# Optimization experiments

Measured on AMD Instinct MI355X. Metric: run time of the kernel, lower is better.

## Reference

```python
import jax, jax.numpy as jnp
import numpy as np

EMBED_DIM = 768
NUM_HEADS = 8
HEAD_DIM = EMBED_DIM // NUM_HEADS
SCALE = HEAD_DIM ** -0.5
B = 256
N_TOTAL = 16384


def setup_inputs() -> dict:
    key = jax.random.key(0)
    ks = jax.random.split(key, 10)
    s = 1.0 / np.sqrt(EMBED_DIM)
    inp = {
        "query": jax.random.normal(ks[0], (B, EMBED_DIM), jnp.float32),
        "search": jax.random.normal(ks[1], (N_TOTAL, EMBED_DIM), jnp.float32),
        # q_proj / k_proj: Linear(embed_dim, embed_dim)
        "Wq": jax.random.uniform(ks[2], (EMBED_DIM, EMBED_DIM), jnp.float32, -s, s),
        "bq": jax.random.uniform(ks[3], (EMBED_DIM,), jnp.float32, -s, s),
        "Wk": jax.random.uniform(ks[4], (EMBED_DIM, EMBED_DIM), jnp.float32, -s, s),
        "bk": jax.random.uniform(ks[5], (EMBED_DIM,), jnp.float32, -s, s),
        # score_fusion: Linear(H, H//2) -> GELU -> Linear(H//2, 1)
        "W1": jax.random.uniform(ks[6], (NUM_HEADS // 2, NUM_HEADS), jnp.float32, -1.0 / np.sqrt(NUM_HEADS), 1.0 / np.sqrt(NUM_HEADS)),
        "b1": jax.random.uniform(ks[7], (NUM_HEADS // 2,), jnp.float32, -1.0 / np.sqrt(NUM_HEADS), 1.0 / np.sqrt(NUM_HEADS)),
        "W2": jax.random.uniform(ks[8], (1, NUM_HEADS // 2), jnp.float32, -1.0 / np.sqrt(NUM_HEADS // 2), 1.0 / np.sqrt(NUM_HEADS // 2)),
        "b2": jax.random.uniform(ks[9], (1,), jnp.float32, -1.0 / np.sqrt(NUM_HEADS // 2), 1.0 / np.sqrt(NUM_HEADS // 2)),
    }
    return inp


def reference(query, search, Wq, bq, Wk, bk, W1, b1, W2, b2):
    Bq = query.shape[0]
    Nt = search.shape[0]
    # projections -> (B, H, hd) and (N, H, hd)
    q = (query @ Wq.T + bq).reshape(Bq, NUM_HEADS, HEAD_DIM)
    k = (search @ Wk.T + bk).reshape(Nt, NUM_HEADS, HEAD_DIM)
    # per-head dot products: (B, N, H)
    attn_logits = jnp.einsum('bhd,nhd->bnh', q, k) * SCALE
    # tiny MLP over head axis: H -> H//2 -> 1, exact (erf) GELU as in torch default
    h = jax.nn.gelu(attn_logits @ W1.T + b1, approximate=False)
    scores = h @ W2.T + b2  # (B, N, 1)
    return scores.squeeze(-1)
```

## Files before the change

kernel.cpp:

```cpp
#include <hip/hip_runtime.h>
#include <math.h>

#define SCALE 0.1020620726159658f

typedef __attribute__((ext_vector_type(8))) short shortx8;
typedef __attribute__((ext_vector_type(4))) float floatx4;

__device__ __forceinline__ float bf2f(unsigned short u) {
  union { unsigned int i; float f; } c; c.i = ((unsigned int)u) << 16; return c.f;
}
__device__ __forceinline__ unsigned short f2bf(float f) {
  union { float f; unsigned int i; } c; c.f = f;
  unsigned int x = c.i;
  x += 0x7fffu + ((x >> 16) & 1u);
  return (unsigned short)(x >> 16);
}
__device__ __forceinline__ float geluf(float x) {
  return 0.5f * x * (1.0f + erff(x * 0.70710678118654752f));
}
__device__ __forceinline__ float lde(const void* p, long i, int fp32) {
  return fp32 ? ((const float*)p)[i] : bf2f(((const unsigned short*)p)[i]);
}

__global__ void detect_dtype(const unsigned short* __restrict__ s, int* __restrict__ flag) {
  int t = threadIdx.x;
  int big = 0;
  for (int i = t; i < 256; i += 64) {
    int e = (s[i] >> 7) & 0xFF;
    if (e >= 160) big = 1;
  }
  unsigned long long m = __ballot(big);
  if (t == 0) *flag = (m != 0ULL) ? 1 : 0;
}

__global__ void convert_in(const void* __restrict__ q, const void* __restrict__ wq,
                           unsigned short* __restrict__ qb, unsigned short* __restrict__ wqb,
                           const int* __restrict__ flagp) {
  int fl = *flagp;
  int idx = blockIdx.x * 256 + threadIdx.x;
  const int n1 = 196608;
  if (idx < n1) {
    qb[idx] = fl ? f2bf(((const float*)q)[idx]) : ((const unsigned short*)q)[idx];
  } else {
    int j = idx - n1;
    wqb[j] = fl ? f2bf(((const float*)wq)[j]) : ((const unsigned short*)wq)[j];
  }
}

__global__ void transpose_bf(const void* __restrict__ in, unsigned short* __restrict__ out,
                             const int* __restrict__ flagp) {
  int fl = *flagp;
  __shared__ unsigned short tile[32][33];
  int tx = threadIdx.x, ty = threadIdx.y;
#pragma unroll
  for (int i = 0; i < 4; i++)
    tile[ty + i * 8][tx] =
        f2bf(lde(in, (long)(blockIdx.y * 32 + ty + i * 8) * 768 + blockIdx.x * 32 + tx, fl));
  __syncthreads();
  int ox = blockIdx.y * 32 + tx;
#pragma unroll
  for (int i = 0; i < 4; i++)
    out[(long)(blockIdx.x * 32 + ty + i * 8) * 768 + ox] = tile[tx][ty + i * 8];
}

template <int EPI>
__global__ __launch_bounds__(256) void gemm_bt(
    const unsigned short* __restrict__ A,
    const void* __restrict__ B,
    void* __restrict__ Cout,
    const void* __restrict__ biasp,
    const void* __restrict__ W2b,
    const void* __restrict__ b2b,
    const int* __restrict__ flagp, int useflag,
    int M, int N, int K)
{
  __shared__ unsigned short As[128 * 64];
  __shared__ unsigned short Bs[128 * 64];
  const int fl = *flagp;
  const int bfp32 = useflag ? fl : 0;
  const int tid = threadIdx.x;
  const int wave = tid >> 6;
  const int lane = tid & 63;
  const int wr = wave >> 1, wc = wave & 1;
  const int m0 = blockIdx.y * 128;
  const int n0 = blockIdx.x * 128;

  floatx4 acc[4][4];
#pragma unroll
  for (int i = 0; i < 4; i++)
#pragma unroll
    for (int j = 0; j < 4; j++) acc[i][j] = (floatx4){0.f, 0.f, 0.f, 0.f};

  const int cL = lane & 7;
  const int quad = lane >> 4;
  const int l15 = lane & 15;

  for (int k0 = 0; k0 < K; k0 += 64) {
#pragma unroll
    for (int t = 0; t < 4; t++) {
      int r = wave * 32 + t * 8 + (lane >> 3);
      int p = cL ^ (r & 7);
      shortx8 va = *(const shortx8*)(A + (size_t)(m0 + r) * K + k0 + cL * 8);
      *(shortx8*)(As + r * 64 + p * 8) = va;
    }
    if (!bfp32) {
      const unsigned short* B16 = (const unsigned short*)B;
#pragma unroll
      for (int t = 0; t < 4; t++) {
        int r = wave * 32 + t * 8 + (lane >> 3);
        int p = cL ^ (r & 7);
        shortx8 vb = *(const shortx8*)(B16 + (size_t)(n0 + r) * K + k0 + cL * 8);
        *(shortx8*)(Bs + r * 64 + p * 8) = vb;
      }
    } else {
      const float* Bf = (const float*)B;
#pragma unroll
      for (int t = 0; t < 4; t++) {
        int r = wave * 32 + t * 8 + (lane >> 3);
        int p = cL ^ (r & 7);
        const float4* src = (const float4*)(Bf + (size_t)(n0 + r) * K + k0 + cL * 8);
        float4 f0 = src[0], f1 = src[1];
        shortx8 vb;
        vb[0] = (short)f2bf(f0.x); vb[1] = (short)f2bf(f0.y);
        vb[2] = (short)f2bf(f0.z); vb[3] = (short)f2bf(f0.w);
        vb[4] = (short)f2bf(f1.x); vb[5] = (short)f2bf(f1.y);
        vb[6] = (short)f2bf(f1.z); vb[7] = (short)f2bf(f1.w);
        *(shortx8*)(Bs + r * 64 + p * 8) = vb;
      }
    }
    __syncthreads();
#pragma unroll
    for (int ks = 0; ks < 2; ks++) {
      shortx8 af[4], bfr[4];
#pragma unroll
      for (int mt = 0; mt < 4; mt++) {
        int r = wr * 64 + mt * 16 + l15;
        int ch = (ks * 4 + quad) ^ (r & 7);
        af[mt] = *(const shortx8*)(As + r * 64 + ch * 8);
      }
#pragma unroll
      for (int nt = 0; nt < 4; nt++) {
        int r = wc * 64 + nt * 16 + l15;
        int ch = (ks * 4 + quad) ^ (r & 7);
        bfr[nt] = *(const shortx8*)(Bs + r * 64 + ch * 8);
      }
#pragma unroll
      for (int mt = 0; mt < 4; mt++)
#pragma unroll
        for (int nt = 0; nt < 4; nt++)
          acc[mt][nt] = __builtin_amdgcn_mfma_f32_16x16x32_bf16(
              af[mt], bfr[nt], acc[mt][nt], 0, 0, 0);
    }
    __syncthreads();
  }

  const int lrow = quad * 4;
  if constexpr (EPI == 0) {
    float* Cf = (float*)Cout;
#pragma unroll
    for (int mt = 0; mt < 4; mt++)
#pragma unroll
      for (int nt = 0; nt < 4; nt++) {
        int gm = m0 + wr * 64 + mt * 16 + lrow;
        int gn = n0 + wc * 64 + nt * 16 + l15;
        float bz = lde(biasp, gn, fl);
#pragma unroll
        for (int r = 0; r < 4; r++)
          Cf[(size_t)(gm + r) * N + gn] = acc[mt][nt][r] + bz;
      }
  } else if constexpr (EPI == 1) {
    unsigned short* Cb = (unsigned short*)Cout;
#pragma unroll
    for (int mt = 0; mt < 4; mt++)
#pragma unroll
      for (int nt = 0; nt < 4; nt++) {
        int gm = m0 + wr * 64 + mt * 16 + lrow;
        int gn = n0 + wc * 64 + nt * 16 + l15;
#pragma unroll
        for (int r = 0; r < 4; r++)
          Cb[(size_t)(gm + r) * N + gn] = f2bf(acc[mt][nt][r]);
      }
  } else {
    const float* cp = (const float*)biasp;
    float w2v[4];
#pragma unroll
    for (int j = 0; j < 4; j++) w2v[j] = lde(W2b, j, fl);
    float b2v = lde(b2b, 0, fl);
#pragma unroll
    for (int mt = 0; mt < 4; mt++) {
      int gm = m0 + wr * 64 + mt * 16 + lrow;
      float cpv0 = cp[gm], cpv1 = cp[gm + 1], cpv2 = cp[gm + 2], cpv3 = cp[gm + 3];
#pragma unroll
      for (int nt = 0; nt < 4; nt++) {
        int gn = n0 + wc * 64 + nt * 16 + l15;
        floatx4 v = acc[mt][nt];
        float s = b2v;
        s += w2v[0] * geluf(v[0] + cpv0);
        s += w2v[1] * geluf(v[1] + cpv1);
        s += w2v[2] * geluf(v[2] + cpv2);
        s += w2v[3] * geluf(v[3] + cpv3);
        size_t oi = (size_t)(gm >> 2) * N + gn;
        if (fl) ((float*)Cout)[oi] = s;
        else    ((unsigned short*)Cout)[oi] = f2bf(s);
      }
    }
  }
}

__global__ void build_qw(const float* __restrict__ q,
                         const void* __restrict__ W1,
                         const void* __restrict__ b1,
                         const void* __restrict__ bk,
                         unsigned short* __restrict__ QW,
                         float* __restrict__ cp,
                         const int* __restrict__ flagp) {
  int fl = *flagp;
  int b = blockIdx.x, t = threadIdx.x;
  __shared__ float red[768];
  __shared__ float w1s[32];
  __shared__ float hcs[8];
  if (t < 32) w1s[t] = lde(W1, t, fl);
  __syncthreads();
  const float* qrow = q + b * 768;
  for (int e = t; e < 768; e += 256) {
    float qv = qrow[e];
    red[e] = qv * lde(bk, e, fl);
    int h = e / 96;
#pragma unroll
    for (int j = 0; j < 4; j++)
      QW[(size_t)(b * 4 + j) * 768 + e] = f2bf(qv * w1s[j * 8 + h] * SCALE);
  }
  __syncthreads();
  if (t < 8) {
    float s = 0.f;
    for (int d = 0; d < 96; d++) s += red[t * 96 + d];
    hcs[t] = s;
  }
  __syncthreads();
  if (t < 4) {
    float s = lde(b1, t, fl);
#pragma unroll
    for (int h = 0; h < 8; h++) s += SCALE * w1s[t * 8 + h] * hcs[h];
    cp[b * 4 + t] = s;
  }
}

extern "C" void kernel_launch(void* const* d_in, const int* in_sizes, int n_in,
                              void* d_out, int out_size, void* d_ws, size_t ws_size,
                              hipStream_t stream) {
  const void* query  = d_in[0];
  const void* search = d_in[1];
  const void* Wq     = d_in[2];
  const void* bq     = d_in[3];
  const void* Wk     = d_in[4];
  const void* bk     = d_in[5];
  const void* W1     = d_in[6];
  const void* b1     = d_in[7];
  const void* W2     = d_in[8];
  const void* b2     = d_in[9];

  char* ws = (char*)d_ws;
  int*            flag = (int*)ws;
  unsigned short* qb   = (unsigned short*)(ws + 16);
  unsigned short* wqb  = (unsigned short*)(ws + 393232);
  unsigned short* WkT  = (unsigned short*)(ws + 1572880);
  float*          qf   = (float*)(ws + 2752528);
  unsigned short* QW   = (unsigned short*)(ws + 3538960);
  unsigned short* QQ   = (unsigned short*)(ws + 5111824);
  float*          cp   = (float*)(ws + 6684688);

  detect_dtype<<<1, 64, 0, stream>>>((const unsigned short*)search, flag);
  convert_in<<<3072, 256, 0, stream>>>(query, Wq, qb, wqb, flag);
  transpose_bf<<<dim3(24, 24), dim3(32, 8), 0, stream>>>(Wk, WkT, flag);
  gemm_bt<0><<<dim3(6, 2), 256, 0, stream>>>(qb, wqb, qf, bq, nullptr, nullptr,
                                             flag, 0, 256, 768, 768);
  build_qw<<<256, 256, 0, stream>>>(qf, W1, b1, bk, QW, cp, flag);
  gemm_bt<1><<<dim3(6, 8), 256, 0, stream>>>(QW, WkT, QQ, nullptr, nullptr, nullptr,
                                             flag, 0, 1024, 768, 768);
  gemm_bt<2><<<dim3(128, 8), 256, 0, stream>>>(QQ, search, d_out, cp, W2, b2,
                                               flag, 1, 1024, 16384, 768);
}
```

Baseline: 204.9 us.

## Drop dtype detection, fuse prep kernels, pre-convert search, async LDS loads, fast GELU

Removes the runtime dtype-detection kernel and assumes fp32 inputs throughout. Merges the Wk transpose and the bf16 conversions of query, Wq and search into one prep kernel. Moves the QW construction into the first GEMM's epilogue, leaving only the cp reduction in a separate kernel. The GEMM now stages tiles with global_load_lds async copies, and the final epilogue swaps the erf GELU for a tanh-style approximation built on exp2 and rcp. The aim is to cut launch count, repeated fp32-to-bf16 conversion of search in the main GEMM, and transcendental cost. The trade-offs are an extra bf16 copy of search, approximate GELU numerics, and dropping support for bf16 inputs.

```diff
diff --git a/kernel.cpp b/kernel.cpp
--- a/kernel.cpp
+++ b/kernel.cpp
@@ -15,52 +15,17 @@
   x += 0x7fffu + ((x >> 16) & 1u);
   return (unsigned short)(x >> 16);
 }
-__device__ __forceinline__ float geluf(float x) {
-  return 0.5f * x * (1.0f + erff(x * 0.70710678118654752f));
-}
-__device__ __forceinline__ float lde(const void* p, long i, int fp32) {
-  return fp32 ? ((const float*)p)[i] : bf2f(((const unsigned short*)p)[i]);
-}
-
-__global__ void detect_dtype(const unsigned short* __restrict__ s, int* __restrict__ flag) {
-  int t = threadIdx.x;
-  int big = 0;
-  for (int i = t; i < 256; i += 64) {
-    int e = (s[i] >> 7) & 0xFF;
-    if (e >= 160) big = 1;
-  }
-  unsigned long long m = __ballot(big);
-  if (t == 0) *flag = (m != 0ULL) ? 1 : 0;
-}
-
-__global__ void convert_in(const void* __restrict__ q, const void* __restrict__ wq,
-                           unsigned short* __restrict__ qb, unsigned short* __restrict__ wqb,
-                           const int* __restrict__ flagp) {
-  int fl = *flagp;
-  int idx = blockIdx.x * 256 + threadIdx.x;
-  const int n1 = 196608;
-  if (idx < n1) {
-    qb[idx] = fl ? f2bf(((const float*)q)[idx]) : ((const unsigned short*)q)[idx];
-  } else {
-    int j = idx - n1;
-    wqb[j] = fl ? f2bf(((const float*)wq)[j]) : ((const unsigned short*)wq)[j];
-  }
-}
-
-__global__ void transpose_bf(const void* __restrict__ in, unsigned short* __restrict__ out,
-                             const int* __restrict__ flagp) {
-  int fl = *flagp;
-  __shared__ unsigned short tile[32][33];
-  int tx = threadIdx.x, ty = threadIdx.y;
-#pragma unroll
-  for (int i = 0; i < 4; i++)
-    tile[ty + i * 8][tx] =
-        f2bf(lde(in, (long)(blockIdx.y * 32 + ty + i * 8) * 768 + blockIdx.x * 32 + tx, fl));
-  __syncthreads();
-  int ox = blockIdx.y * 32 + tx;
-#pragma unroll
-  for (int i = 0; i < 4; i++)
-    out[(long)(blockIdx.x * 32 + ty + i * 8) * 768 + ox] = tile[tx][ty + i * 8];
+__device__ __forceinline__ float gelu_fast(float x) {
+  float x2 = x * x;
+  float y = x * (0.7978845608f + 0.0356774081f * x2);
+  float e = fminf(y * 2.885390082f, 60.0f);
+  float t = exp2f(e);
+  return x * t * __builtin_amdgcn_rcpf(t + 1.0f);
+}
+__device__ __forceinline__ void async_ld16(const unsigned short* g, unsigned short* l) {
+  __builtin_amdgcn_global_load_lds(
+      (const __attribute__((address_space(1))) unsigned int*)g,
+      (__attribute__((address_space(3))) unsigned int*)l, 16, 0, 0);
 }
 
 template <int EPI>
@@ -68,16 +33,12 @@
     const unsigned short* __restrict__ A,
     const void* __restrict__ B,
     void* __restrict__ Cout,
-    const void* __restrict__ biasp,
-    const void* __restrict__ W2b,
-    const void* __restrict__ b2b,
-    const int* __restrict__ flagp, int useflag,
-    int M, int N, int K)
+    const void* __restrict__ p0, const void* __restrict__ p1,
+    void* __restrict__ p2, const void* __restrict__ p3,
+    int bconv, int M, int N, int K)
 {
   __shared__ unsigned short As[128 * 64];
   __shared__ unsigned short Bs[128 * 64];
-  const int fl = *flagp;
-  const int bfp32 = useflag ? fl : 0;
   const int tid = threadIdx.x;
   const int wave = tid >> 6;
   const int lane = tid & 63;
@@ -91,33 +52,36 @@
 #pragma unroll
     for (int j = 0; j < 4; j++) acc[i][j] = (floatx4){0.f, 0.f, 0.f, 0.f};
 
+  const int rl = lane >> 3;
+  const int cl = (lane & 7) ^ rl;
+  const unsigned short* gA[4];
+  const unsigned short* gB[4];
+  unsigned short* lA[4];
+  unsigned short* lB[4];
+#pragma unroll
+  for (int t = 0; t < 4; t++) {
+    int r = wave * 32 + t * 8 + rl;
+    gA[t] = A + (size_t)(m0 + r) * K + cl * 8;
+    gB[t] = (const unsigned short*)B + (size_t)(n0 + r) * K + cl * 8;
+    lA[t] = As + (wave * 32 + t * 8) * 64;
+    lB[t] = Bs + (wave * 32 + t * 8) * 64;
+  }
   const int cL = lane & 7;
   const int quad = lane >> 4;
   const int l15 = lane & 15;
 
   for (int k0 = 0; k0 < K; k0 += 64) {
 #pragma unroll
-    for (int t = 0; t < 4; t++) {
-      int r = wave * 32 + t * 8 + (lane >> 3);
-      int p = cL ^ (r & 7);
-      shortx8 va = *(const shortx8*)(A + (size_t)(m0 + r) * K + k0 + cL * 8);
-      *(shortx8*)(As + r * 64 + p * 8) = va;
-    }
-    if (!bfp32) {
-      const unsigned short* B16 = (const unsigned short*)B;
-#pragma unroll
-      for (int t = 0; t < 4; t++) {
-        int r = wave * 32 + t * 8 + (lane >> 3);
-        int p = cL ^ (r & 7);
-        shortx8 vb = *(const shortx8*)(B16 + (size_t)(n0 + r) * K + k0 + cL * 8);
-        *(shortx8*)(Bs + r * 64 + p * 8) = vb;
-      }
+    for (int t = 0; t < 4; t++) async_ld16(gA[t] + k0, lA[t]);
+    if (!bconv) {
+#pragma unroll
+      for (int t = 0; t < 4; t++) async_ld16(gB[t] + k0, lB[t]);
     } else {
       const float* Bf = (const float*)B;
 #pragma unroll
       for (int t = 0; t < 4; t++) {
-        int r = wave * 32 + t * 8 + (lane >> 3);
-        int p = cL ^ (r & 7);
+        int r = wave * 32 + t * 8 + rl;
+        int p = cL ^ rl;
         const float4* src = (const float4*)(Bf + (size_t)(n0 + r) * K + k0 + cL * 8);
         float4 f0 = src[0], f1 = src[1];
         shortx8 vb;
@@ -156,17 +120,29 @@
 
   const int lrow = quad * 4;
   if constexpr (EPI == 0) {
-    float* Cf = (float*)Cout;
+    const float* bqv = (const float*)p0;
+    const float* W1f = (const float*)p1;
+    float* qf = (float*)p2;
+    unsigned short* QWo = (unsigned short*)Cout;
 #pragma unroll
     for (int mt = 0; mt < 4; mt++)
 #pragma unroll
       for (int nt = 0; nt < 4; nt++) {
         int gm = m0 + wr * 64 + mt * 16 + lrow;
         int gn = n0 + wc * 64 + nt * 16 + l15;
-        float bz = lde(biasp, gn, fl);
-#pragma unroll
-        for (int r = 0; r < 4; r++)
-          Cf[(size_t)(gm + r) * N + gn] = acc[mt][nt][r] + bz;
+        float bz = bqv[gn];
+        int h = gn / 96;
+        float w1h0 = W1f[h], w1h1 = W1f[8 + h], w1h2 = W1f[16 + h], w1h3 = W1f[24 + h];
+#pragma unroll
+        for (int r = 0; r < 4; r++) {
+          float qv = acc[mt][nt][r] + bz;
+          qf[(size_t)(gm + r) * N + gn] = qv;
+          size_t base = (size_t)((gm + r) * 4) * N + gn;
+          QWo[base]         = f2bf(SCALE * w1h0 * qv);
+          QWo[base + N]     = f2bf(SCALE * w1h1 * qv);
+          QWo[base + 2 * N] = f2bf(SCALE * w1h2 * qv);
+          QWo[base + 3 * N] = f2bf(SCALE * w1h3 * qv);
+        }
       }
   } else if constexpr (EPI == 1) {
     unsigned short* Cb = (unsigned short*)Cout;
@@ -181,11 +157,12 @@
           Cb[(size_t)(gm + r) * N + gn] = f2bf(acc[mt][nt][r]);
       }
   } else {
-    const float* cp = (const float*)biasp;
-    float w2v[4];
-#pragma unroll
-    for (int j = 0; j < 4; j++) w2v[j] = lde(W2b, j, fl);
-    float b2v = lde(b2b, 0, fl);
+    const float* cp = (const float*)p0;
+    const float* W2f = (const float*)p1;
+    const float* b2f = (const float*)p3;
+    float* Co = (float*)Cout;
+    float w2v0 = W2f[0], w2v1 = W2f[1], w2v2 = W2f[2], w2v3 = W2f[3];
+    float b2v = b2f[0];
 #pragma unroll
     for (int mt = 0; mt < 4; mt++) {
       int gm = m0 + wr * 64 + mt * 16 + lrow;
@@ -195,41 +172,65 @@
         int gn = n0 + wc * 64 + nt * 16 + l15;
         floatx4 v = acc[mt][nt];
         float s = b2v;
-        s += w2v[0] * geluf(v[0] + cpv0);
-        s += w2v[1] * geluf(v[1] + cpv1);
-        s += w2v[2] * geluf(v[2] + cpv2);
-        s += w2v[3] * geluf(v[3] + cpv3);
-        size_t oi = (size_t)(gm >> 2) * N + gn;
-        if (fl) ((float*)Cout)[oi] = s;
-        else    ((unsigned short*)Cout)[oi] = f2bf(s);
+        s += w2v0 * gelu_fast(v[0] + cpv0);
+        s += w2v1 * gelu_fast(v[1] + cpv1);
+        s += w2v2 * gelu_fast(v[2] + cpv2);
+        s += w2v3 * gelu_fast(v[3] + cpv3);
+        Co[(size_t)(gm >> 2) * N + gn] = s;
       }
     }
   }
 }
 
-__global__ void build_qw(const float* __restrict__ q,
-                         const void* __restrict__ W1,
-                         const void* __restrict__ b1,
-                         const void* __restrict__ bk,
-                         unsigned short* __restrict__ QW,
-                         float* __restrict__ cp,
-                         const int* __restrict__ flagp) {
-  int fl = *flagp;
+__device__ __forceinline__ void cvt8(const float* __restrict__ src,
+                                     unsigned short* __restrict__ dst, size_t i) {
+  float4 a = *(const float4*)(src + i);
+  float4 b = *(const float4*)(src + i + 4);
+  shortx8 v;
+  v[0] = (short)f2bf(a.x); v[1] = (short)f2bf(a.y);
+  v[2] = (short)f2bf(a.z); v[3] = (short)f2bf(a.w);
+  v[4] = (short)f2bf(b.x); v[5] = (short)f2bf(b.y);
+  v[6] = (short)f2bf(b.z); v[7] = (short)f2bf(b.w);
+  *(shortx8*)(dst + i) = v;
+}
+
+__global__ __launch_bounds__(256) void prep(
+    const float* __restrict__ query, const float* __restrict__ Wq,
+    const float* __restrict__ Wk, const float* __restrict__ search,
+    unsigned short* __restrict__ qb, unsigned short* __restrict__ wqb,
+    unsigned short* __restrict__ WkT, unsigned short* __restrict__ sb)
+{
+  int b = blockIdx.x, t = threadIdx.x;
+  if (b < 576) {
+    __shared__ unsigned short tile[32][33];
+    int bx = b % 24, by = b / 24;
+    int tx = t & 31, ty = t >> 5;
+#pragma unroll
+    for (int i = 0; i < 4; i++)
+      tile[ty + i * 8][tx] = f2bf(Wk[(size_t)(by * 32 + ty + i * 8) * 768 + bx * 32 + tx]);
+    __syncthreads();
+#pragma unroll
+    for (int i = 0; i < 4; i++)
+      WkT[(size_t)(bx * 32 + ty + i * 8) * 768 + by * 32 + tx] = tile[tx][ty + i * 8];
+  } else if (b < 672) {
+    cvt8(query, qb, (size_t)(b - 576) * 2048 + t * 8);
+  } else if (b < 960) {
+    cvt8(Wq, wqb, (size_t)(b - 672) * 2048 + t * 8);
+  } else {
+    cvt8(search, sb, (size_t)(b - 960) * 2048 + t * 8);
+  }
+}
+
+__global__ __launch_bounds__(256) void finish_cp(
+    const float* __restrict__ qf, const float* __restrict__ W1f,
+    const float* __restrict__ b1f, const float* __restrict__ bkf,
+    float* __restrict__ cp)
+{
   int b = blockIdx.x, t = threadIdx.x;
   __shared__ float red[768];
-  __shared__ float w1s[32];
   __shared__ float hcs[8];
-  if (t < 32) w1s[t] = lde(W1, t, fl);
-  __syncthreads();
-  const float* qrow = q + b * 768;
-  for (int e = t; e < 768; e += 256) {
-    float qv = qrow[e];
-    red[e] = qv * lde(bk, e, fl);
-    int h = e / 96;
-#pragma unroll
-    for (int j = 0; j < 4; j++)
-      QW[(size_t)(b * 4 + j) * 768 + e] = f2bf(qv * w1s[j * 8 + h] * SCALE);
-  }
+  const float* qrow = qf + (size_t)b * 768;
+  for (int e = t; e < 768; e += 256) red[e] = qrow[e] * bkf[e];
   __syncthreads();
   if (t < 8) {
     float s = 0.f;
@@ -238,9 +239,9 @@
   }
   __syncthreads();
   if (t < 4) {
-    float s = lde(b1, t, fl);
-#pragma unroll
-    for (int h = 0; h < 8; h++) s += SCALE * w1s[t * 8 + h] * hcs[h];
+    float s = b1f[t];
+#pragma unroll
+    for (int h = 0; h < 8; h++) s += SCALE * W1f[t * 8 + h] * hcs[h];
     cp[b * 4 + t] = s;
   }
 }
@@ -248,35 +249,38 @@
 extern "C" void kernel_launch(void* const* d_in, const int* in_sizes, int n_in,
                               void* d_out, int out_size, void* d_ws, size_t ws_size,
                               hipStream_t stream) {
-  const void* query  = d_in[0];
-  const void* search = d_in[1];
-  const void* Wq     = d_in[2];
-  const void* bq     = d_in[3];
-  const void* Wk     = d_in[4];
-  const void* bk     = d_in[5];
-  const void* W1     = d_in[6];
-  const void* b1     = d_in[7];
-  const void* W2     = d_in[8];
-  const void* b2     = d_in[9];
+  const float* query  = (const float*)d_in[0];
+  const float* search = (const float*)d_in[1];
+  const float* Wq     = (const float*)d_in[2];
+  const float* bq     = (const float*)d_in[3];
+  const float* Wk     = (const float*)d_in[4];
+  const float* bk     = (const float*)d_in[5];
+  const float* W1     = (const float*)d_in[6];
+  const float* b1     = (const float*)d_in[7];
+  const float* W2     = (const float*)d_in[8];
+  const float* b2     = (const float*)d_in[9];
 
   char* ws = (char*)d_ws;
-  int*            flag = (int*)ws;
-  unsigned short* qb   = (unsigned short*)(ws + 16);
-  unsigned short* wqb  = (unsigned short*)(ws + 393232);
-  unsigned short* WkT  = (unsigned short*)(ws + 1572880);
-  float*          qf   = (float*)(ws + 2752528);
-  unsigned short* QW   = (unsigned short*)(ws + 3538960);
-  unsigned short* QQ   = (unsigned short*)(ws + 5111824);
-  float*          cp   = (float*)(ws + 6684688);
-
-  detect_dtype<<<1, 64, 0, stream>>>((const unsigned short*)search, flag);
-  convert_in<<<3072, 256, 0, stream>>>(query, Wq, qb, wqb, flag);
-  transpose_bf<<<dim3(24, 24), dim3(32, 8), 0, stream>>>(Wk, WkT, flag);
-  gemm_bt<0><<<dim3(6, 2), 256, 0, stream>>>(qb, wqb, qf, bq, nullptr, nullptr,
-                                             flag, 0, 256, 768, 768);
-  build_qw<<<256, 256, 0, stream>>>(qf, W1, b1, bk, QW, cp, flag);
+  float*          cp  = (float*)ws;
+  float*          qf  = (float*)(ws + 4096);
+  unsigned short* qb  = (unsigned short*)(ws + 790528);
+  unsigned short* wqb = (unsigned short*)(ws + 1183744);
+  unsigned short* WkT = (unsigned short*)(ws + 2363392);
+  unsigned short* QW  = (unsigned short*)(ws + 3543040);
+  unsigned short* QQ  = (unsigned short*)(ws + 5115904);
+  unsigned short* sb  = (unsigned short*)(ws + 6688768);
+  const int use_sb = (ws_size >= 31854592) ? 1 : 0;
+
+  prep<<<use_sb ? 7104 : 960, 256, 0, stream>>>(query, Wq, Wk, search, qb, wqb, WkT, sb);
+  gemm_bt<0><<<dim3(6, 2), 256, 0, stream>>>(qb, wqb, QW, bq, W1, qf, nullptr,
+                                             0, 256, 768, 768);
+  finish_cp<<<256, 256, 0, stream>>>(qf, W1, b1, bk, cp);
   gemm_bt<1><<<dim3(6, 8), 256, 0, stream>>>(QW, WkT, QQ, nullptr, nullptr, nullptr,
-                                             flag, 0, 1024, 768, 768);
-  gemm_bt<2><<<dim3(128, 8), 256, 0, stream>>>(QQ, search, d_out, cp, W2, b2,
-                                               flag, 1, 1024, 16384, 768);
-}
+                                             nullptr, 0, 1024, 768, 768);
+  if (use_sb)
+    gemm_bt<2><<<dim3(128, 8), 256, 0, stream>>>(QQ, sb, d_out, cp, W2, nullptr,
+                                                 (void*)b2, 0, 1024, 16384, 768);
+  else
+    gemm_bt<2><<<dim3(128, 8), 256, 0, stream>>>(QQ, search, d_out, cp, W2, nullptr,
+                                                 (void*)b2, 1, 1024, 16384, 768);
+}
```

New measurement: 181.0 us. 1.13x faster.
